# Kernel tuning notes

Hardware: AMD Instinct MI355X
Metric: run time of the kernel (lower is better)

The kernel has to match this reference:

```python
import math
import jax, jax.numpy as jnp
import numpy as np

B, N, C, H = 64, 197, 768, 12
KEEP_RATE = 0.7

def setup_inputs() -> dict:
    key = jax.random.key(0)
    k0, k1, k2 = jax.random.split(key, 3)
    x = jax.random.normal(k0, (B, N, C), jnp.float32)
    qkv_w = jax.random.normal(k1, (C, 3 * C), jnp.float32) * 0.02
    qkv_b = jnp.zeros((3 * C,), jnp.float32)
    proj_w = jax.random.normal(k2, (C, C), jnp.float32) * 0.02
    proj_b = jnp.zeros((C,), jnp.float32)
    return {"x": x, "qkv_w": qkv_w, "qkv_b": qkv_b, "proj_w": proj_w, "proj_b": proj_b}

def reference(x, qkv_w, qkv_b, proj_w, proj_b):
    b, n, c = x.shape
    d = c // H
    scale = d ** -0.5
    # qkv: [B,N,3C] -> [3,B,H,N,d]
    qkv = (x @ qkv_w + qkv_b).reshape(b, n, 3, H, d)
    qkv = jnp.transpose(qkv, (2, 0, 3, 1, 4))
    q, k, v = qkv[0], qkv[1], qkv[2]
    attn = jax.nn.softmax(jnp.einsum('bhnd,bhmd->bhnm', q, k) * scale, axis=-1)  # [B,H,N,N]
    out = jnp.einsum('bhnm,bhmd->bhnd', attn, v)          # [B,H,N,d]
    out = jnp.transpose(out, (0, 2, 1, 3)).reshape(b, n, c)
    x_out = out @ proj_w + proj_b                          # [B,N,C]
    # dynamic token pruning via CLS attention (row 0, excluding CLS itself)
    left_tokens = math.ceil(KEEP_RATE * (n - 1))
    cls_attn = attn[:, :, 0, 1:].mean(axis=1)              # [B,N-1]
    _, idx = jax.lax.top_k(cls_attn, left_tokens)          # descending, sorted
    index = jnp.broadcast_to(idx[:, :, None], (b, left_tokens, c))
    return (x_out, index, idx, cls_attn, left_tokens)
```

## Files before the change

### kernel.cpp

```cpp
#include <hip/hip_runtime.h>
#include <math.h>

#define BB   64
#define NTOK 197
#define CC   768
#define HH   12
#define DH   64
#define MTOT (BB * NTOK)
#define MPAD 12672
#define LEFT 138

#define XOUT_OFF  0
#define INDEX_OFF 9682944
#define IDX_OFF   16465920
#define CLS_OFF   16474752
#define LT_OFF    16487296

typedef short s8v __attribute__((ext_vector_type(8)));
typedef short s4v __attribute__((ext_vector_type(4)));
typedef float f4v __attribute__((ext_vector_type(4)));

#define GLOAD16(g, l) __builtin_amdgcn_global_load_lds( \
    (const __attribute__((address_space(1))) unsigned int*)(g), \
    (__attribute__((address_space(3))) unsigned int*)(l), 16, 0, 0)

__device__ __forceinline__ unsigned short f2bf(float f) {
    union { float f; unsigned int i; } x; x.f = f;
    unsigned int r = x.i + 0x7FFFu + ((x.i >> 16) & 1u);
    return (unsigned short)(r >> 16);
}

__global__ __launch_bounds__(256)
void convert_x(const float* __restrict__ in, unsigned short* __restrict__ outb)
{
    size_t i = ((size_t)blockIdx.x * 256 + threadIdx.x) * 8;
    float4 a = *(const float4*)(in + i);
    float4 b = *(const float4*)(in + i + 4);
    s8v r;
    r[0] = (short)f2bf(a.x); r[1] = (short)f2bf(a.y);
    r[2] = (short)f2bf(a.z); r[3] = (short)f2bf(a.w);
    r[4] = (short)f2bf(b.x); r[5] = (short)f2bf(b.y);
    r[6] = (short)f2bf(b.z); r[7] = (short)f2bf(b.w);
    *(s8v*)(outb + i) = r;
}

__global__ __launch_bounds__(256)
void transpose_w2(const float* __restrict__ inq, const float* __restrict__ inp,
                  unsigned short* __restrict__ outq, unsigned short* __restrict__ outp)
{
    __shared__ float tile[32][33];
    const int bi = blockIdx.x;
    int bj = blockIdx.y;
    const float* in; unsigned short* outb; int N;
    if (bj < 72) { in = inq; outb = outq; N = 2304; }
    else         { bj -= 72; in = inp; outb = outp; N = 768; }
    const int tx = threadIdx.x & 31, ty = threadIdx.x >> 5;
#pragma unroll
    for (int r = ty; r < 32; r += 8)
        tile[r][tx] = in[(size_t)(bi * 32 + r) * N + bj * 32 + tx];
    __syncthreads();
#pragma unroll
    for (int r = ty; r < 32; r += 8)
        outb[(size_t)(bj * 32 + r) * 768 + bi * 32 + tx] = f2bf(tile[tx][r]);
}

__global__ __launch_bounds__(256, 3)
void gemm_bf16(const unsigned short* __restrict__ A, const unsigned short* __restrict__ BT,
               const float* __restrict__ bias, int ncolt, int mode,
               unsigned short* __restrict__ outb, float* __restrict__ outf)
{
    const int id = blockIdx.x;
    const int xcd = id & 7;
    const int t = id >> 3;
    const int ct = t % ncolt, s = t / ncolt;
    const int rt = s * 8 + xcd;
    if (rt >= 99) return;
    const int m0 = rt * 128, n0 = ct * 128;

    const int tid = threadIdx.x;
    const int wave = tid >> 6, lane = tid & 63;
    const int quad = lane >> 4, l16 = lane & 15;
    const int rowbase = (wave >> 1) * 64, colbase = (wave & 1) * 64;
    __shared__ __align__(16) short As[128 * 64];
    __shared__ __align__(16) short Bs[128 * 64];

    const int rA   = lane >> 3;
    const int gcol = ((lane & 7) ^ rA) * 8;
    unsigned int agof[4], bgof[4];
#pragma unroll
    for (int i = 0; i < 4; ++i) {
        int c = wave * 4 + i;
        agof[i] = (unsigned int)((m0 + c * 8 + rA) * 768 + gcol);
        bgof[i] = (unsigned int)((n0 + c * 8 + rA) * 768 + gcol);
    }
    int aoff[4], boff[4];
#pragma unroll
    for (int i = 0; i < 4; ++i) {
        aoff[i] = (rowbase + i * 16 + l16) * 64 + ((quad ^ (l16 & 7)) * 8);
        boff[i] = (colbase + i * 16 + l16) * 64 + ((quad ^ (l16 & 7)) * 8);
    }

    f4v acc[4][4];
#pragma unroll
    for (int i = 0; i < 4; ++i)
#pragma unroll
        for (int j = 0; j < 4; ++j) acc[i][j] = (f4v)0.f;

    for (int k0 = 0; k0 < 768; k0 += 64) {
#pragma unroll
        for (int i = 0; i < 4; ++i) {
            int c = wave * 4 + i;
            GLOAD16(A  + agof[i] + k0, &As[c * 512]);
            GLOAD16(BT + bgof[i] + k0, &Bs[c * 512]);
        }
        __syncthreads();
#pragma unroll
        for (int ks = 0; ks < 2; ++ks) {
            const int x = ks * 32;
            s8v af[4], bf[4];
#pragma unroll
            for (int i = 0; i < 4; ++i) af[i] = *(const s8v*)&As[aoff[i] ^ x];
#pragma unroll
            for (int j = 0; j < 4; ++j) bf[j] = *(const s8v*)&Bs[boff[j] ^ x];
#pragma unroll
            for (int i = 0; i < 4; ++i)
#pragma unroll
                for (int j = 0; j < 4; ++j)
                    acc[i][j] = __builtin_amdgcn_mfma_f32_16x16x32_bf16(bf[j], af[i], acc[i][j], 0, 0, 0);
        }
        __syncthreads();
    }

    const int ncols = mode ? 768 : 2304;
#pragma unroll
    for (int i = 0; i < 4; ++i) {
        const int m = m0 + rowbase + i * 16 + l16;
        if (m >= MTOT) continue;
#pragma unroll
        for (int j = 0; j < 4; ++j) {
            const int nb = n0 + colbase + j * 16 + quad * 4;
            float4 b4 = *(const float4*)&bias[nb];
            if (mode == 1) {
                float4 r;
                r.x = acc[i][j][0] + b4.x; r.y = acc[i][j][1] + b4.y;
                r.z = acc[i][j][2] + b4.z; r.w = acc[i][j][3] + b4.w;
                *(float4*)(outf + (size_t)m * ncols + nb) = r;
            } else {
                s4v r;
                r[0] = (short)f2bf(acc[i][j][0] + b4.x);
                r[1] = (short)f2bf(acc[i][j][1] + b4.y);
                r[2] = (short)f2bf(acc[i][j][2] + b4.z);
                r[3] = (short)f2bf(acc[i][j][3] + b4.w);
                *(s4v*)(outb + (size_t)m * ncols + nb) = r;
            }
        }
    }
}

#define VTS 224

__global__ __launch_bounds__(256)
void transpose_v(const unsigned short* __restrict__ qkv, unsigned short* __restrict__ vt)
{
    __shared__ short tile[32][33];
    const int bx = blockIdx.x;
    const int by = blockIdx.y;
    const int bh = blockIdx.z;
    const int b = bh / HH, h = bh - b * HH;
    const int tx = threadIdx.x & 31, ty = threadIdx.x >> 5;
    const unsigned short* vin = qkv + (size_t)b * NTOK * 2304 + 1536 + h * DH;
#pragma unroll
    for (int r = ty; r < 32; r += 8) {
        const int tok = bx * 32 + r;
        tile[r][tx] = (tok < NTOK) ? (short)vin[(size_t)tok * 2304 + by * 32 + tx] : (short)0;
    }
    __syncthreads();
#pragma unroll
    for (int r = ty; r < 32; r += 8) {
        const int d = by * 32 + r;
        vt[((size_t)bh * DH + d) * VTS + bx * 32 + tx] = tile[tx][r];
    }
}

#define PSTR 226
#define AW   5
#define ATH  320

__global__ __launch_bounds__(ATH)
void attn_mfma(const unsigned short* __restrict__ qkv, const unsigned short* __restrict__ vt,
               unsigned short* __restrict__ attnbf)
{
    const int bh = blockIdx.x;
    const int b = bh / HH, h = bh - b * HH;
    const int tid = threadIdx.x;
    const int wave = tid >> 6, lane = tid & 63;
    const int quad = lane >> 4, l16 = lane & 15;
    __shared__ short Ps[AW][16 * PSTR];

    const unsigned short* qg = qkv + (size_t)b * NTOK * 2304 + h * DH;
    const unsigned short* kg = qg + 768;
    const unsigned short* vtb = vt + (size_t)bh * DH * VTS;

    for (int strip = wave; strip < 13; strip += AW) {
        const int mq = min(strip * 16 + l16, NTOK - 1);
        const s8v aq0 = *(const s8v*)(qg + (size_t)mq * 2304 + quad * 8);
        const s8v aq1 = *(const s8v*)(qg + (size_t)mq * 2304 + 32 + quad * 8);

        f4v sacc[14];
#pragma unroll
        for (int j = 0; j < 14; ++j) sacc[j] = (f4v)0.f;
        __builtin_amdgcn_s_setprio(1);
#pragma unroll
        for (int j = 0; j < 14; ++j) {
            const int kt = min(j * 16 + l16, NTOK - 1);
            s8v bk0 = *(const s8v*)(kg + (size_t)kt * 2304 + quad * 8);
            s8v bk1 = *(const s8v*)(kg + (size_t)kt * 2304 + 32 + quad * 8);
            sacc[j] = __builtin_amdgcn_mfma_f32_16x16x32_bf16(bk0, aq0, sacc[j], 0, 0, 0);
            sacc[j] = __builtin_amdgcn_mfma_f32_16x16x32_bf16(bk1, aq1, sacc[j], 0, 0, 0);
        }
        __builtin_amdgcn_s_setprio(0);

        float mx = -1e30f;
#pragma unroll
        for (int j = 0; j < 14; ++j)
#pragma unroll
            for (int r = 0; r < 4; ++r) {
                const int key = j * 16 + quad * 4 + r;
                float s = (key < NTOK) ? sacc[j][r] * 0.125f : -1e30f;
                sacc[j][r] = s;
                mx = fmaxf(mx, s);
            }
        mx = fmaxf(mx, __shfl_xor(mx, 16, 64));
        mx = fmaxf(mx, __shfl_xor(mx, 32, 64));

        float sm = 0.f;
#pragma unroll
        for (int j = 0; j < 14; ++j) {
            s4v pk;
#pragma unroll
            for (int r = 0; r < 4; ++r) {
                const int key = j * 16 + quad * 4 + r;
                float p = (key < NTOK) ? __expf(sacc[j][r] - mx) : 0.f;
                sm += p;
                pk[r] = (short)f2bf(p);
            }
            *(s4v*)&Ps[wave][l16 * PSTR + j * 16 + quad * 4] = pk;
        }
        sm += __shfl_xor(sm, 16, 64);
        sm += __shfl_xor(sm, 32, 64);
        const float rcp = 1.f / sm;

        f4v oacc[4];
#pragma unroll
        for (int j = 0; j < 4; ++j) oacc[j] = (f4v)0.f;
        __builtin_amdgcn_s_setprio(1);
#pragma unroll
        for (int t = 0; t < 7; ++t) {
            const int ko = t * 32 + quad * 8;
            s8v ap = *(const s8v*)&Ps[wave][l16 * PSTR + ko];
#pragma unroll
            for (int j = 0; j < 4; ++j) {
                s8v bv = *(const s8v*)(vtb + (size_t)(j * 16 + l16) * VTS + ko);
                oacc[j] = __builtin_amdgcn_mfma_f32_16x16x32_bf16(bv, ap, oacc[j], 0, 0, 0);
            }
        }
        __builtin_amdgcn_s_setprio(0);
        const int qrow = strip * 16 + l16;
        if (qrow < NTOK) {
#pragma unroll
            for (int j = 0; j < 4; ++j) {
                s4v o4;
#pragma unroll
                for (int r = 0; r < 4; ++r) o4[r] = (short)f2bf(oacc[j][r] * rcp);
                *(s4v*)&attnbf[((size_t)b * NTOK + qrow) * 768 + h * DH + j * 16 + quad * 4] = o4;
            }
        }
    }
}

#define QCH  64
#define BGRP 8

__global__ __launch_bounds__(256)
void qr_kernel(const float* __restrict__ x, const float* __restrict__ qkv_w,
               const float* __restrict__ qkv_b, float* __restrict__ rws,
               float* __restrict__ bconst)
{
    const int h  = blockIdx.x;
    const int b0 = blockIdx.y * BGRP;
    const int tid = threadIdx.x;
    __shared__ float x0s[BGRP][CC];
    __shared__ float wbuf[2][QCH * DH];
    __shared__ float q0s[BGRP][DH];

    for (int u = tid; u < BGRP * CC; u += 256) {
        int b = u / CC, c = u - b * CC;
        x0s[b][c] = x[(size_t)(b0 + b) * NTOK * CC + c];
    }
    for (int u = tid; u < QCH * DH; u += 256) {
        int cc = u >> 6, dd = u & 63;
        wbuf[0][u] = qkv_w[(size_t)cc * 2304 + h * DH + dd];
    }
    __syncthreads();

    const int d  = tid & 63;
    const int bA = tid >> 6;
    const int bB = bA + 4;
    float accA = qkv_b[h * DH + d];
    float accB = qkv_b[h * DH + d];
    for (int k = 0; k < CC / QCH; ++k) {
        const int cur = k & 1;
        if (k + 1 < CC / QCH) {
            const int cbase = (k + 1) * QCH;
            for (int u = tid; u < QCH * DH; u += 256) {
                int cc = u >> 6, dd = u & 63;
                wbuf[cur ^ 1][u] = qkv_w[(size_t)(cbase + cc) * 2304 + h * DH + dd];
            }
        }
        const int cb = k * QCH;
#pragma unroll
        for (int cc = 0; cc < QCH; ++cc) {
            const float wv = wbuf[cur][cc * 64 + d];
            accA = fmaf(x0s[bA][cb + cc], wv, accA);
            accB = fmaf(x0s[bB][cb + cc], wv, accB);
        }
        __syncthreads();
    }
    q0s[bA][d] = accA;
    q0s[bB][d] = accB;
    __syncthreads();

    if (tid < BGRP) {
        float acc3 = 0.f;
        for (int dd = 0; dd < DH; ++dd) acc3 += q0s[tid][dd] * qkv_b[CC + h * DH + dd];
        bconst[(b0 + tid) * HH + h] = acc3;
    }

    for (int c = tid; c < CC; c += 256) {
        const float* wrow = qkv_w + (size_t)c * 2304 + CC + h * DH;
        float acc2[BGRP];
#pragma unroll
        for (int b = 0; b < BGRP; ++b) acc2[b] = 0.f;
#pragma unroll
        for (int dd = 0; dd < DH; dd += 4) {
            float4 w4 = *(const float4*)(wrow + dd);
#pragma unroll
            for (int b = 0; b < BGRP; ++b) {
                acc2[b] = fmaf(w4.x, q0s[b][dd + 0], acc2[b]);
                acc2[b] = fmaf(w4.y, q0s[b][dd + 1], acc2[b]);
                acc2[b] = fmaf(w4.z, q0s[b][dd + 2], acc2[b]);
                acc2[b] = fmaf(w4.w, q0s[b][dd + 3], acc2[b]);
            }
        }
#pragma unroll
        for (int b = 0; b < BGRP; ++b)
            rws[((size_t)(b0 + b) * HH + h) * CC + c] = acc2[b];
    }
}

__global__ __launch_bounds__(256)
void cls_s(const float* __restrict__ x, const float* __restrict__ rws,
           const float* __restrict__ bconst, float* __restrict__ sws)
{
    const int b = blockIdx.y;
    const int tid = threadIdx.x;
    __shared__ __align__(16) float rl[HH * 772];
    __shared__ float bcs[HH];
#pragma unroll
    for (int h = 0; h < HH; ++h)
        for (int c = tid; c < CC; c += 256)
            rl[h * 772 + c] = rws[((size_t)b * HH + h) * CC + c];
    if (tid < HH) bcs[tid] = bconst[b * HH + tid];
    __syncthreads();
    const int local = blockIdx.x * 256 + tid;
    if (local < NTOK * HH) {
        const int tok = local / HH;
        const int h = local - tok * HH;
        const float* xr = x + ((size_t)b * NTOK + tok) * CC;
        const float* rp = rl + h * 772;
        float acc = 0.f;
#pragma unroll 8
        for (int c = 0; c < CC; c += 4) {
            float4 x4 = *(const float4*)(xr + c);
            float4 r4 = *(const float4*)(rp + c);
            acc = fmaf(x4.x, r4.x, acc);
            acc = fmaf(x4.y, r4.y, acc);
            acc = fmaf(x4.z, r4.z, acc);
            acc = fmaf(x4.w, r4.w, acc);
        }
        sws[((size_t)b * HH + h) * NTOK + tok] = (acc + bcs[h]) * 0.125f;
    }
}

__global__ __launch_bounds__(256)
void cls_topk(const float* __restrict__ sws, float* __restrict__ out, int write_lt)
{
    const int b = blockIdx.x, tid = threadIdx.x;
    const int wave = tid >> 6, lane = tid & 63;
    __shared__ float sbuf[HH][208];
    __shared__ float pm[4][208];
    __shared__ float vals[256];
    __shared__ int   idxs[256];

    for (int jj = lane; jj < 208; jj += 64) pm[wave][jj] = 0.f;
    if (tid < NTOK) {
#pragma unroll
        for (int h = 0; h < HH; ++h)
            sbuf[h][tid] = sws[((size_t)b * HH + h) * NTOK + tid];
    }
    __syncthreads();

    for (int h = wave; h < HH; h += 4) {
        float sv[4], ev[4];
        float mx = -1e30f;
#pragma unroll
        for (int t = 0; t < 4; ++t) {
            int j = lane + 64 * t;
            sv[t] = (j < NTOK) ? sbuf[h][j] : -1e30f;
            mx = fmaxf(mx, sv[t]);
        }
#pragma unroll
        for (int off = 1; off < 64; off <<= 1) mx = fmaxf(mx, __shfl_xor(mx, off, 64));
        float sm = 0.f;
#pragma unroll
        for (int t = 0; t < 4; ++t) {
            int j = lane + 64 * t;
            ev[t] = (j < NTOK) ? expf(sv[t] - mx) : 0.f;
            sm += ev[t];
        }
#pragma unroll
        for (int off = 1; off < 64; off <<= 1) sm += __shfl_xor(sm, off, 64);
#pragma unroll
        for (int t = 0; t < 4; ++t) {
            int j = lane + 64 * t;
            if (j < NTOK) pm[wave][j] += ev[t] / sm;
        }
    }
    __syncthreads();

    float v = -INFINITY;
    int id = 256 + tid;
    if (tid < NTOK - 1) {
        int j = tid + 1;
        float s = ((pm[0][j] + pm[1][j]) + (pm[2][j] + pm[3][j])) * (1.f / 12.f);
        v = s; id = tid;
        out[CLS_OFF + (size_t)b * (NTOK - 1) + tid] = s;
    }
    vals[tid] = v; idxs[tid] = id;
    __syncthreads();

    for (int k = 2; k <= 256; k <<= 1) {
        for (int j = k >> 1; j > 0; j >>= 1) {
            int ixj = tid ^ j;
            if (ixj > tid) {
                float va = vals[tid], vb2 = vals[ixj];
                int ia = idxs[tid], ib = idxs[ixj];
                bool aLess = (va > vb2) || (va == vb2 && ia < ib);
                bool dir = ((tid & k) == 0);
                if (dir != aLess) {
                    vals[tid] = vb2; vals[ixj] = va;
                    idxs[tid] = ib;  idxs[ixj] = ia;
                }
            }
            __syncthreads();
        }
    }

    if (tid < LEFT) out[IDX_OFF + (size_t)b * LEFT + tid] = (float)idxs[tid];
    if (write_lt && b == 0 && tid == 0) out[LT_OFF] = (float)LEFT;
}

__global__ __launch_bounds__(64)
void write_index(const float* __restrict__ idx_in, float* __restrict__ out)
{
    const int row = blockIdx.x;
    const float v = idx_in[row];
    const int tid = threadIdx.x;
    float4 r; r.x = v; r.y = v; r.z = v; r.w = v;
#pragma unroll
    for (int i = 0; i < 3; ++i)
        *(float4*)(out + INDEX_OFF + (size_t)row * CC + (tid + 64 * i) * 4) = r;
}

extern "C" void kernel_launch(void* const* d_in, const int* in_sizes, int n_in,
                              void* d_out, int out_size, void* d_ws, size_t ws_size,
                              hipStream_t stream)
{
    const float* x      = (const float*)d_in[0];
    const float* qkv_w  = (const float*)d_in[1];
    const float* qkv_b  = (const float*)d_in[2];
    const float* proj_w = (const float*)d_in[3];
    const float* proj_b = (const float*)d_in[4];
    float* out = (float*)d_out;

    char* w = (char*)d_ws;
    unsigned short* xbf   = (unsigned short*)w; w += (size_t)MPAD * CC * 2;
    unsigned short* wt1   = (unsigned short*)w; w += (size_t)3 * CC * CC * 2;
    unsigned short* wt2   = (unsigned short*)w; w += (size_t)CC * CC * 2;
    unsigned short* qkvbf = (unsigned short*)w; w += (size_t)MTOT * 3 * CC * 2;
    unsigned short* atbf  = (unsigned short*)w; w += (size_t)MPAD * CC * 2;
    float* rws    = (float*)w; w += (size_t)BB * HH * CC * 4;
    float* bconst = (float*)w; w += (size_t)BB * HH * 4;
    float* sws    = (float*)w; w += (size_t)BB * HH * NTOK * 4;
    unsigned short* vtbf  = (unsigned short*)d_ws;

    convert_x<<<dim3(4728), 256, 0, stream>>>(x, xbf);
    transpose_w2<<<dim3(24, 96), 256, 0, stream>>>(qkv_w, proj_w, wt1, wt2);
    qr_kernel<<<dim3(HH, BB / BGRP), 256, 0, stream>>>(x, qkv_w, qkv_b, rws, bconst);
    cls_s<<<dim3(10, 64), 256, 0, stream>>>(x, rws, bconst, sws);
    cls_topk<<<dim3(BB), 256, 0, stream>>>(sws, out, (out_size > LT_OFF) ? 1 : 0);
    write_index<<<dim3(BB * LEFT), 64, 0, stream>>>(out + IDX_OFF, out);
    gemm_bf16<<<dim3(8 * 18 * 13), 256, 0, stream>>>(xbf, wt1, qkv_b, 18, 0, qkvbf, nullptr);
    transpose_v<<<dim3(7, 2, BB * HH), 256, 0, stream>>>(qkvbf, vtbf);
    attn_mfma<<<dim3(BB * HH), ATH, 0, stream>>>(qkvbf, vtbf, atbf);
    gemm_bf16<<<dim3(8 * 6 * 13), 256, 0, stream>>>(atbf, wt2, proj_b, 6, 1,
                                                    nullptr, out + XOUT_OFF);
}
```

Before: 363.5 us.

## Stage K in swizzled LDS and split attention query strips across blocks

The attention kernel now launches four blocks per (batch, head), each with four waves handling one 16-row query strip, instead of one block looping five waves over 13 strips. The full K tile for the head is loaded cooperatively into XOR-swizzled shared memory so QK^T reads come from LDS rather than strided global loads. V^T fragments are prefetched into registers before the softmax to hide global latency. In exchange each block reloads all of K redundantly, and the register-held V fragments raise register pressure; some waves in the last group do no compute.

```diff
diff --git a/kernel.cpp b/kernel.cpp
--- a/kernel.cpp
+++ b/kernel.cpp
@@ -183,97 +183,112 @@
 }
 
 #define PSTR 226
-#define AW   5
-#define ATH  320
-
-__global__ __launch_bounds__(ATH)
-void attn_mfma(const unsigned short* __restrict__ qkv, const unsigned short* __restrict__ vt,
-               unsigned short* __restrict__ attnbf)
+
+__global__ __launch_bounds__(256, 2)
+void attn_mfma4(const unsigned short* __restrict__ qkv, const unsigned short* __restrict__ vt,
+                unsigned short* __restrict__ attnbf)
 {
     const int bh = blockIdx.x;
+    const int g  = blockIdx.y;
     const int b = bh / HH, h = bh - b * HH;
     const int tid = threadIdx.x;
     const int wave = tid >> 6, lane = tid & 63;
     const int quad = lane >> 4, l16 = lane & 15;
-    __shared__ short Ps[AW][16 * PSTR];
+    __shared__ __align__(16) short Ks[NTOK * 64];
+    __shared__ short Ps[4][16 * PSTR];
 
     const unsigned short* qg = qkv + (size_t)b * NTOK * 2304 + h * DH;
     const unsigned short* kg = qg + 768;
     const unsigned short* vtb = vt + (size_t)bh * DH * VTS;
 
-    for (int strip = wave; strip < 13; strip += AW) {
-        const int mq = min(strip * 16 + l16, NTOK - 1);
-        const s8v aq0 = *(const s8v*)(qg + (size_t)mq * 2304 + quad * 8);
-        const s8v aq1 = *(const s8v*)(qg + (size_t)mq * 2304 + 32 + quad * 8);
-
-        f4v sacc[14];
-#pragma unroll
-        for (int j = 0; j < 14; ++j) sacc[j] = (f4v)0.f;
-        __builtin_amdgcn_s_setprio(1);
-#pragma unroll
-        for (int j = 0; j < 14; ++j) {
-            const int kt = min(j * 16 + l16, NTOK - 1);
-            s8v bk0 = *(const s8v*)(kg + (size_t)kt * 2304 + quad * 8);
-            s8v bk1 = *(const s8v*)(kg + (size_t)kt * 2304 + 32 + quad * 8);
-            sacc[j] = __builtin_amdgcn_mfma_f32_16x16x32_bf16(bk0, aq0, sacc[j], 0, 0, 0);
-            sacc[j] = __builtin_amdgcn_mfma_f32_16x16x32_bf16(bk1, aq1, sacc[j], 0, 0, 0);
-        }
-        __builtin_amdgcn_s_setprio(0);
-
-        float mx = -1e30f;
-#pragma unroll
-        for (int j = 0; j < 14; ++j)
-#pragma unroll
-            for (int r = 0; r < 4; ++r) {
-                const int key = j * 16 + quad * 4 + r;
-                float s = (key < NTOK) ? sacc[j][r] * 0.125f : -1e30f;
-                sacc[j][r] = s;
-                mx = fmaxf(mx, s);
-            }
-        mx = fmaxf(mx, __shfl_xor(mx, 16, 64));
-        mx = fmaxf(mx, __shfl_xor(mx, 32, 64));
-
-        float sm = 0.f;
-#pragma unroll
-        for (int j = 0; j < 14; ++j) {
-            s4v pk;
-#pragma unroll
-            for (int r = 0; r < 4; ++r) {
-                const int key = j * 16 + quad * 4 + r;
-                float p = (key < NTOK) ? __expf(sacc[j][r] - mx) : 0.f;
-                sm += p;
-                pk[r] = (short)f2bf(p);
-            }
-            *(s4v*)&Ps[wave][l16 * PSTR + j * 16 + quad * 4] = pk;
-        }
-        sm += __shfl_xor(sm, 16, 64);
-        sm += __shfl_xor(sm, 32, 64);
-        const float rcp = 1.f / sm;
-
-        f4v oacc[4];
-#pragma unroll
-        for (int j = 0; j < 4; ++j) oacc[j] = (f4v)0.f;
-        __builtin_amdgcn_s_setprio(1);
-#pragma unroll
-        for (int t = 0; t < 7; ++t) {
-            const int ko = t * 32 + quad * 8;
-            s8v ap = *(const s8v*)&Ps[wave][l16 * PSTR + ko];
-#pragma unroll
-            for (int j = 0; j < 4; ++j) {
-                s8v bv = *(const s8v*)(vtb + (size_t)(j * 16 + l16) * VTS + ko);
-                oacc[j] = __builtin_amdgcn_mfma_f32_16x16x32_bf16(bv, ap, oacc[j], 0, 0, 0);
-            }
-        }
-        __builtin_amdgcn_s_setprio(0);
-        const int qrow = strip * 16 + l16;
-        if (qrow < NTOK) {
-#pragma unroll
-            for (int j = 0; j < 4; ++j) {
-                s4v o4;
-#pragma unroll
-                for (int r = 0; r < 4; ++r) o4[r] = (short)f2bf(oacc[j][r] * rcp);
-                *(s4v*)&attnbf[((size_t)b * NTOK + qrow) * 768 + h * DH + j * 16 + quad * 4] = o4;
-            }
+    for (int u = tid; u < NTOK * 8; u += 256) {
+        const int row = u >> 3, seg = u & 7;
+        *(s8v*)&Ks[row * 64 + (seg ^ (row & 7)) * 8] =
+            *(const s8v*)(kg + (size_t)row * 2304 + seg * 8);
+    }
+    __syncthreads();
+
+    const int strip = g * 4 + wave;
+    if (strip >= 13) return;
+
+    const int mq = min(strip * 16 + l16, NTOK - 1);
+    const s8v aq0 = *(const s8v*)(qg + (size_t)mq * 2304 + quad * 8);
+    const s8v aq1 = *(const s8v*)(qg + (size_t)mq * 2304 + 32 + quad * 8);
+
+    f4v sacc[14];
+#pragma unroll
+    for (int j = 0; j < 14; ++j) sacc[j] = (f4v)0.f;
+    __builtin_amdgcn_s_setprio(1);
+#pragma unroll
+    for (int j = 0; j < 14; ++j) {
+        const int kt = min(j * 16 + l16, NTOK - 1);
+        s8v bk0 = *(const s8v*)&Ks[kt * 64 + ((quad       ^ (kt & 7)) * 8)];
+        s8v bk1 = *(const s8v*)&Ks[kt * 64 + (((quad + 4) ^ (kt & 7)) * 8)];
+        sacc[j] = __builtin_amdgcn_mfma_f32_16x16x32_bf16(bk0, aq0, sacc[j], 0, 0, 0);
+        sacc[j] = __builtin_amdgcn_mfma_f32_16x16x32_bf16(bk1, aq1, sacc[j], 0, 0, 0);
+    }
+    __builtin_amdgcn_s_setprio(0);
+
+    s8v bvr[7][4];
+#pragma unroll
+    for (int t = 0; t < 7; ++t) {
+        const int ko = t * 32 + quad * 8;
+#pragma unroll
+        for (int j = 0; j < 4; ++j)
+            bvr[t][j] = *(const s8v*)(vtb + (size_t)(j * 16 + l16) * VTS + ko);
+    }
+
+    float mx = -1e30f;
+#pragma unroll
+    for (int j = 0; j < 14; ++j)
+#pragma unroll
+        for (int r = 0; r < 4; ++r) {
+            const int key = j * 16 + quad * 4 + r;
+            float s = (key < NTOK) ? sacc[j][r] * 0.125f : -1e30f;
+            sacc[j][r] = s;
+            mx = fmaxf(mx, s);
+        }
+    mx = fmaxf(mx, __shfl_xor(mx, 16, 64));
+    mx = fmaxf(mx, __shfl_xor(mx, 32, 64));
+
+    float sm = 0.f;
+#pragma unroll
+    for (int j = 0; j < 14; ++j) {
+        s4v pk;
+#pragma unroll
+        for (int r = 0; r < 4; ++r) {
+            const int key = j * 16 + quad * 4 + r;
+            float p = (key < NTOK) ? __expf(sacc[j][r] - mx) : 0.f;
+            sm += p;
+            pk[r] = (short)f2bf(p);
+        }
+        *(s4v*)&Ps[wave][l16 * PSTR + j * 16 + quad * 4] = pk;
+    }
+    sm += __shfl_xor(sm, 16, 64);
+    sm += __shfl_xor(sm, 32, 64);
+    const float rcp = 1.f / sm;
+
+    f4v oacc[4];
+#pragma unroll
+    for (int j = 0; j < 4; ++j) oacc[j] = (f4v)0.f;
+    __builtin_amdgcn_s_setprio(1);
+#pragma unroll
+    for (int t = 0; t < 7; ++t) {
+        const int ko = t * 32 + quad * 8;
+        s8v ap = *(const s8v*)&Ps[wave][l16 * PSTR + ko];
+#pragma unroll
+        for (int j = 0; j < 4; ++j)
+            oacc[j] = __builtin_amdgcn_mfma_f32_16x16x32_bf16(bvr[t][j], ap, oacc[j], 0, 0, 0);
+    }
+    __builtin_amdgcn_s_setprio(0);
+    const int qrow = strip * 16 + l16;
+    if (qrow < NTOK) {
+#pragma unroll
+        for (int j = 0; j < 4; ++j) {
+            s4v o4;
+#pragma unroll
+            for (int r = 0; r < 4; ++r) o4[r] = (short)f2bf(oacc[j][r] * rcp);
+            *(s4v*)&attnbf[((size_t)b * NTOK + qrow) * 768 + h * DH + j * 16 + quad * 4] = o4;
         }
     }
 }
@@ -512,7 +527,7 @@
     write_index<<<dim3(BB * LEFT), 64, 0, stream>>>(out + IDX_OFF, out);
     gemm_bf16<<<dim3(8 * 18 * 13), 256, 0, stream>>>(xbf, wt1, qkv_b, 18, 0, qkvbf, nullptr);
     transpose_v<<<dim3(7, 2, BB * HH), 256, 0, stream>>>(qkvbf, vtbf);
-    attn_mfma<<<dim3(BB * HH), ATH, 0, stream>>>(qkvbf, vtbf, atbf);
+    attn_mfma4<<<dim3(BB * HH, 4), 256, 0, stream>>>(qkvbf, vtbf, atbf);
     gemm_bf16<<<dim3(8 * 6 * 13), 256, 0, stream>>>(atbf, wt2, proj_b, 6, 1,
                                                     nullptr, out + XOUT_OFF);
 }
```

Measured after the change: 342.7 us. 1.06x faster.
